# Kernel optimization log

Measured on AMD Instinct MI355X. Metric: run time of the kernel, lower is better.

The kernel has to match this reference:

```python
import jax, jax.numpy as jnp
import numpy as np
from jax import lax


def _make_inds(n):
    # Indices of the inner n x n grid inside the (n+2) x (n+2) channel grid
    # (matches the torch module, which assumes kk == 1).
    ci = np.arange(n * n, dtype=np.int64).reshape(n, n)
    ci = ci + 1 + np.arange(n, dtype=np.int64)[:, None] * 2
    ci = ci + n + 2
    return jnp.asarray(ci.reshape(-1))


def setup_inputs() -> dict:
    key = jax.random.key(0)
    k1, _ = jax.random.split(key)
    n, kk = 14, 1
    n_in = n + 2 * kk
    B, H, W = 32, 64, 64
    x = jax.random.normal(k1, (B, n_in * n_in, H, W), dtype=jnp.float32)
    weight = jnp.ones((1,), dtype=jnp.float32)
    return {"x": x, "weight": weight, "n": n, "kk": kk}


def reference(x, weight, n, kk):
    B, C, H, W = x.shape
    n_in = n + 2 * kk
    win = 2 * kk + 1
    inds = _make_inds(n)

    valid_x = x[:, inds]  # [B, n^2, H, W]

    # exp(detach(x) * weight): gradient is blocked through x here
    xexp = jnp.exp(lax.stop_gradient(x) * weight[0])  # [B, n_in^2, H, W]

    # Windowed channel-grid sum: instead of the dense 1x1 conv with a mostly
    # zero [n^2, n_in^2] weight, do a (2kk+1)x(2kk+1) sliding-window sum over
    # the channel grid directly.
    grid = xexp.reshape(B, n_in, n_in, H * W)
    sums = lax.reduce_window(grid, jnp.float32(0), lax.add,
                             (1, win, win, 1), (1, 1, 1, 1), "VALID")
    denom = sums.reshape(B, n * n, H, W)

    imp = xexp[:, inds] / denom
    return valid_x * imp
```

## Files before the change

### kernel.cpp

```cpp
#include <hip/hip_runtime.h>
#include <hip/hip_bf16.h>


#define NIN 16
#define NOUT 14
#define HW 4096

__global__ __launch_bounds__(256) void fc_kernel(
    const float* __restrict__ x,
    const float* __restrict__ wp,
    float* __restrict__ out)
{
    const float w = wp[0];
    const int hw = blockIdx.x * blockDim.x + threadIdx.x;
    const int b  = blockIdx.y;

    const float* xb = x   + ((size_t)b * (NIN * NIN)) * HW + hw;
    float*       ob = out + ((size_t)b * (NOUT * NOUT)) * HW + hw;

    float eA[NIN], eB[NIN], eC[NIN];
    float xB[NIN], xC[NIN];

    #pragma unroll
    for (int c = 0; c < NIN; ++c) {
        float v = xb[(size_t)c * HW];
        eA[c] = __expf(v * w);
    }
    #pragma unroll
    for (int c = 0; c < NIN; ++c) {
        float v = xb[(size_t)(NIN + c) * HW];
        xB[c] = v;
        eB[c] = __expf(v * w);
    }

    for (int i = 0; i < NOUT; ++i) {
        #pragma unroll
        for (int c = 0; c < NIN; ++c) {
            float v = xb[(size_t)((i + 2) * NIN + c) * HW];
            xC[c] = v;
            eC[c] = __expf(v * w);
        }

        float cs[NIN];
        #pragma unroll
        for (int c = 0; c < NIN; ++c) cs[c] = eA[c] + eB[c] + eC[c];

        #pragma unroll
        for (int j = 0; j < NOUT; ++j) {
            float denom = cs[j] + cs[j + 1] + cs[j + 2];
            float num   = xB[j + 1] * eB[j + 1];
            ob[(size_t)(i * NOUT + j) * HW] = __fdividef(num, denom);
        }

        #pragma unroll
        for (int c = 0; c < NIN; ++c) {
            eA[c] = eB[c];
            eB[c] = eC[c];
            xB[c] = xC[c];
        }
    }
}

extern "C" void kernel_launch(void* const* d_in, const int* in_sizes, int n_in,
                              void* d_out, int out_size, void* d_ws, size_t ws_size,
                              hipStream_t stream) {
    const float* x  = (const float*)d_in[0];
    const float* wp = (const float*)d_in[1];
    float* out = (float*)d_out;

    dim3 block(256, 1, 1);
    dim3 grid(HW / 256, 32, 1);
    hipLaunchKernelGGL(fc_kernel, grid, block, 0, stream, x, wp, out);
}
```

Measured before the change: 49.68 us.

## Parallelize output rows across grid instead of sliding window per thread

Each thread now computes one output row i (selected by blockIdx.y) rather than looping over all 14 rows with a rolling three-row register window. This raises the grid from 512 blocks to 7168 blocks, giving many more waves in flight to hide memory latency on a bandwidth-bound kernel. The cost is recomputation: each input row is loaded and exponentiated up to three times instead of once, which raises global read traffic, though L2 or MALL may absorb much of it.

Result: no change. 48.79 us (-1.8%).

```diff
diff --git a/kernel.cpp b/kernel.cpp
--- a/kernel.cpp
+++ b/kernel.cpp
@@ -13,51 +13,37 @@
 {
     const float w = wp[0];
     const int hw = blockIdx.x * blockDim.x + threadIdx.x;
-    const int b  = blockIdx.y;
+    const int i  = blockIdx.y;
+    const int b  = blockIdx.z;
 
-    const float* xb = x   + ((size_t)b * (NIN * NIN)) * HW + hw;
-    float*       ob = out + ((size_t)b * (NOUT * NOUT)) * HW + hw;
+    const float* xb = x + ((size_t)(b * (NIN * NIN) + i * NIN)) * HW + hw;
 
-    float eA[NIN], eB[NIN], eC[NIN];
-    float xB[NIN], xC[NIN];
+    float cs[NIN];
+    float num[NIN];
 
     #pragma unroll
     for (int c = 0; c < NIN; ++c) {
         float v = xb[(size_t)c * HW];
-        eA[c] = __expf(v * w);
+        cs[c] = __expf(v * w);
     }
     #pragma unroll
     for (int c = 0; c < NIN; ++c) {
         float v = xb[(size_t)(NIN + c) * HW];
-        xB[c] = v;
-        eB[c] = __expf(v * w);
+        float e = __expf(v * w);
+        cs[c] += e;
+        num[c] = v * e;
+    }
+    #pragma unroll
+    for (int c = 0; c < NIN; ++c) {
+        float v = xb[(size_t)(2 * NIN + c) * HW];
+        cs[c] += __expf(v * w);
     }
 
-    for (int i = 0; i < NOUT; ++i) {
-        #pragma unroll
-        for (int c = 0; c < NIN; ++c) {
-            float v = xb[(size_t)((i + 2) * NIN + c) * HW];
-            xC[c] = v;
-            eC[c] = __expf(v * w);
-        }
-
-        float cs[NIN];
-        #pragma unroll
-        for (int c = 0; c < NIN; ++c) cs[c] = eA[c] + eB[c] + eC[c];
-
-        #pragma unroll
-        for (int j = 0; j < NOUT; ++j) {
-            float denom = cs[j] + cs[j + 1] + cs[j + 2];
-            float num   = xB[j + 1] * eB[j + 1];
-            ob[(size_t)(i * NOUT + j) * HW] = __fdividef(num, denom);
-        }
-
-        #pragma unroll
-        for (int c = 0; c < NIN; ++c) {
-            eA[c] = eB[c];
-            eB[c] = eC[c];
-            xB[c] = xC[c];
-        }
+    float* ob = out + ((size_t)(b * (NOUT * NOUT) + i * NOUT)) * HW + hw;
+    #pragma unroll
+    for (int j = 0; j < NOUT; ++j) {
+        float denom = cs[j] + cs[j + 1] + cs[j + 2];
+        ob[(size_t)j * HW] = __fdividef(num[j + 1], denom);
     }
 }
 
@@ -69,6 +55,6 @@
     float* out = (float*)d_out;
 
     dim3 block(256, 1, 1);
-    dim3 grid(HW / 256, 32, 1);
+    dim3 grid(HW / 256, NOUT, 32);
     hipLaunchKernelGGL(fc_kernel, grid, block, 0, stream, x, wp, out);
 }
```
